# Optimization experiments

Measured on AMD Instinct MI355X. Metric: run time of the kernel, lower is better.

Reference implementation:

```python
import jax, jax.numpy as jnp
import numpy as np

B, P, H, D, CLASSES, L = 2048, 1024, 2048, 256, 10, 10
EP = 1e-64
LOG2PI = float(np.log(2.0 * np.pi))


def setup_inputs() -> dict:
    key = jax.random.key(0)
    ks = jax.random.split(key, 16)
    s = 0.05
    return {
        "data": jax.random.normal(ks[0], (B, P), dtype=jnp.float32),
        "mask": jax.random.randint(ks[1], (B, P), 0, 2) > 0,
        "enc_w1": jax.random.normal(ks[2], (P, H), dtype=jnp.float32) * s,
        "enc_b1": jnp.zeros((H,), jnp.float32),
        "enc_w2": jax.random.normal(ks[3], (H, 2 * D), dtype=jnp.float32) * s,
        "enc_b2": jnp.zeros((2 * D,), jnp.float32),
        "dec_w1": jax.random.normal(ks[4], (D, H), dtype=jnp.float32) * s,
        "dec_b1": jnp.zeros((H,), jnp.float32),
        "dec_w2": jax.random.normal(ks[5], (H, 3 * P), dtype=jnp.float32) * s,
        "dec_b2": jnp.zeros((3 * P,), jnp.float32),
        "cls_w1": jax.random.normal(ks[6], (P, H), dtype=jnp.float32) * s,
        "cls_b1": jnp.zeros((H,), jnp.float32),
        "cls_w2": jax.random.normal(ks[7], (H, CLASSES), dtype=jnp.float32) * s,
        "cls_b2": jnp.zeros((CLASSES,), jnp.float32),
    }


def _student_t_logprob(x, loc, scale, df):
    y = (x - loc) / scale
    return (jax.lax.lgamma((df + 1.0) * 0.5) - jax.lax.lgamma(df * 0.5)
            - 0.5 * jnp.log(df * jnp.pi) - jnp.log(scale)
            - 0.5 * (df + 1.0) * jnp.log1p(y * y / df))


def reference(data, mask, enc_w1, enc_b1, enc_w2, enc_b2,
              dec_w1, dec_b1, dec_w2, dec_b2,
              cls_w1, cls_b1, cls_w2, cls_b2):
    maskf = mask.astype(data.dtype)
    key = jax.random.key(42)
    k_eps, k_t = jax.random.split(key)

    # encoder
    he = jax.nn.relu(data @ enc_w1 + enc_b1)
    out_enc = he @ enc_w2 + enc_b2                      # [B, 2D]
    mu, sig = out_enc[:, :D], jax.nn.softplus(out_enc[:, D:]) + EP

    # reparameterized q(z|x) samples, L draws
    eps = jax.random.normal(k_eps, (L, B, D), dtype=data.dtype)
    z = mu[None] + sig[None] * eps                      # [L, B, D]
    zf = z.reshape(L * B, D)

    # decoder -> StudentT params
    hd = jax.nn.relu(zf @ dec_w1 + dec_b1)
    out_dec = hd @ dec_w2 + dec_b2                      # [L*B, 3P]
    means = out_dec[:, :P]
    scales = jax.nn.softplus(out_dec[:, P:2 * P]) + 0.001
    dfree = jax.nn.softplus(out_dec[:, 2 * P:]) + 3.0

    data_t = jnp.tile(data, (L, 1))                     # [L*B, P]
    mask_t = jnp.tile(maskf, (L, 1))
    logpx = _student_t_logprob(data_t, means, scales, dfree)
    logpxobs = jnp.sum(logpx * mask_t, axis=1).reshape(L, B)

    logpz = jnp.sum(-0.5 * z * z, axis=-1) - 0.5 * D * LOG2PI          # [L, B]
    logq = jnp.sum(-0.5 * eps * eps - jnp.log(sig)[None], axis=-1) - 0.5 * D * LOG2PI

    imp_w = jax.nn.softmax(logpxobs + logpz - logq, axis=0)            # [L, B]

    # non-reparameterized StudentT sample (torch .sample() is detached)
    t = jax.random.t(k_t, dfree, shape=dfree.shape)
    xms = jax.lax.stop_gradient(means + scales * t).reshape(L, B, P)
    xm = jnp.einsum('ki,kij->ij', imp_w, xms)

    data_imputed = jnp.where(mask, data, xm)
    hc = jax.nn.relu(data_imputed @ cls_w1 + cls_b1)
    logits = hc @ cls_w2 + cls_b2
    return (data_imputed, logits)
```

## Files before the change

kernel.cpp:

```cpp
#include <hip/hip_runtime.h>
#include <math.h>

typedef unsigned int u32;
typedef unsigned short u16;
typedef __attribute__((ext_vector_type(8))) short bf16x8;
typedef __attribute__((ext_vector_type(16))) float f32x16;

struct U2 { u32 a, b; };

__host__ __device__ __forceinline__ U2 tf2x32(u32 k0, u32 k1, u32 c0, u32 c1) {
  u32 ks2 = k0 ^ k1 ^ 0x1BD11BDAu;
  u32 x0 = c0 + k0, x1 = c1 + k1;
#define TFR(r) { x0 += x1; x1 = (x1 << (r)) | (x1 >> (32 - (r))); x1 ^= x0; }
  TFR(13) TFR(15) TFR(26) TFR(6)
  x0 += k1; x1 += ks2 + 1u;
  TFR(17) TFR(29) TFR(16) TFR(24)
  x0 += ks2; x1 += k0 + 2u;
  TFR(13) TFR(15) TFR(26) TFR(6)
  x0 += k0; x1 += k1 + 3u;
  TFR(17) TFR(29) TFR(16) TFR(24)
  x0 += k1; x1 += ks2 + 4u;
  TFR(13) TFR(15) TFR(26) TFR(6)
  x0 += ks2; x1 += k0 + 5u;
#undef TFR
  return {x0, x1};
}

__host__ __device__ __forceinline__ u32 prf32(u32 k0, u32 k1, u32 i) {
  U2 r = tf2x32(k0, k1, 0u, i);
  return r.a ^ r.b;
}

__device__ __forceinline__ float u01_from_bits(u32 bits) {
  u32 r = (bits >> 9) | 0x3f800000u;
  return __uint_as_float(r) - 1.0f;
}

__device__ __forceinline__ float erfinv_f32(float x) {
  float w = -log1pf(-x * x);
  float p;
  if (w < 5.0f) {
    w -= 2.5f;
    p = 2.81022636e-08f;
    p = fmaf(p, w, 3.43273939e-07f);
    p = fmaf(p, w, -3.5233877e-06f);
    p = fmaf(p, w, -4.39150654e-06f);
    p = fmaf(p, w, 0.00021858087f);
    p = fmaf(p, w, -0.00125372503f);
    p = fmaf(p, w, -0.00417768164f);
    p = fmaf(p, w, 0.246640727f);
    p = fmaf(p, w, 1.50140941f);
  } else {
    w = sqrtf(w) - 3.0f;
    p = -0.000200214257f;
    p = fmaf(p, w, 0.000100950558f);
    p = fmaf(p, w, 0.00134934322f);
    p = fmaf(p, w, -0.00367342844f);
    p = fmaf(p, w, 0.00573950773f);
    p = fmaf(p, w, -0.0076224613f);
    p = fmaf(p, w, 0.00943887047f);
    p = fmaf(p, w, 1.00167406f);
    p = fmaf(p, w, 2.83297682f);
  }
  return p * x;
}

__device__ __forceinline__ float normal_from_bits(u32 bits) {
  const float lo = -0.99999994f;
  float u = u01_from_bits(bits) * 2.0f + lo;
  u = fmaxf(lo, u);
  return 1.41421356237f * erfinv_f32(u);
}

__device__ __forceinline__ float softplus_f(float x) {
  return fmaxf(x, 0.0f) + log1pf(expf(-fabsf(x)));
}

struct GI { bool acc; float V; u32 k0, k1; };
__device__ __forceinline__ GI gamma_iter(u32 k0, u32 k1, float d, float c) {
  U2 nk = tf2x32(k0, k1, 0u, 0u);
  U2 xk = tf2x32(k0, k1, 0u, 1u);
  U2 uk = tf2x32(k0, k1, 0u, 2u);
  u32 xk0 = xk.a, xk1 = xk.b;
  float x, v;
  do {
    U2 nxt = tf2x32(xk0, xk1, 0u, 0u);
    U2 sub = tf2x32(xk0, xk1, 0u, 1u);
    xk0 = nxt.a; xk1 = nxt.b;
    x = normal_from_bits(prf32(sub.a, sub.b, 0u));
    v = 1.0f + x * c;
  } while (v <= 0.0f);
  float X = x * x;
  float V = (v * v) * v;
  float U = u01_from_bits(prf32(uk.a, uk.b, 0u));
  bool cont = (U >= 1.0f - 0.0331f * (X * X)) &&
              (logf(U) >= 0.5f * X + d * ((1.0f - V) + logf(V)));
  GI r; r.acc = !cont; r.V = V; r.k0 = nk.a; r.k1 = nk.b;
  return r;
}

__device__ __forceinline__ float lgamma_half_diff(float x) {
  float z = x + 3.0f;
  float num = x * (x + 1.0f) * (x + 2.0f);
  float den = (x + 0.5f) * (x + 1.5f) * (x + 2.5f);
  float zh = z + 0.5f;
  float iz = 1.0f / z, izh = 1.0f / zh;
  float corr = 0.0833333333f * (izh - iz)
             - 0.00277777778f * (izh * izh * izh - iz * iz * iz);
  return logf(num / den) + 0.5f * logf(z) + z * log1pf(0.5f * iz) - 0.5f + corr;
}

__device__ __forceinline__ u16 f2bf(float f) {
  u32 u = __float_as_uint(f);
  u32 r = ((u >> 16) & 1u) + 0x7fffu;
  return (u16)((u + r) >> 16);
}
__device__ __forceinline__ float bf2f(u16 h) { return __uint_as_float(((u32)h) << 16); }

__device__ __forceinline__ void split2(float v, u16& h, u16& m) {
  h = f2bf(v);
  m = f2bf(v - bf2f(h));
}

#define GLOAD16(gp, lp) __builtin_amdgcn_global_load_lds( \
    (const __attribute__((address_space(1))) void*)(gp),  \
    (__attribute__((address_space(3))) void*)(lp), 16, 0, 0)

template<bool RELU, bool SIX, bool SWZ>
__global__ __launch_bounds__(256, 4) void gemm_s3(const u16* __restrict__ A2,
                                                  const u16* __restrict__ B2T,
                                                  const float* __restrict__ bias,
                                                  float* __restrict__ Cf,
                                                  u16* __restrict__ C2,
                                                  int N, int kbits) {
  __shared__ u16 As[128 * 64];
  __shared__ u16 Bs[128 * 64];
  const int tid = threadIdx.x;
  const int l = tid & 63, w = tid >> 6;
  int bx = blockIdx.x, by = blockIdx.y;
  if (SWZ) {
    int nx = gridDim.x;
    int wg = by * nx + bx;
    int per = (nx * gridDim.y) >> 3;
    int sw = (wg & 7) * per + (wg >> 3);
    bx = sw % nx; by = sw / nx;
  }
  const int m0 = by * 128, n0 = bx * 128;
  const int K2 = 2 << kbits;
  const int srow = l >> 3;
  const int scol = ((l & 7) ^ srow) << 3;
  const u16* agr[4]; const u16* bgr[4]; u16* al[4]; u16* bl[4];
#pragma unroll
  for (int j = 0; j < 4; ++j) {
    int r = w * 32 + j * 8 + srow;
    agr[j] = A2 + (size_t)(m0 + r) * K2 + scol;
    bgr[j] = B2T + (size_t)(n0 + r) * K2 + scol;
    al[j] = &As[(w * 4 + j) * 512];
    bl[j] = &Bs[(w * 4 + j) * 512];
  }
  f32x16 acc[2][2] = {};
  const int fr = l & 31;
  const int wm = w >> 1, wn = w & 1;
  const int swz = (l & 7) << 4;
  const int hk16 = (l >> 5) << 4;
  const int nk = 3 << (kbits - 6);
  const int kmask = (1 << kbits) - 1;
  for (int kt = 0; kt < nk; ++kt) {
    int vb = kt << 6;
    int s = vb >> kbits;
    int ko = vb & kmask;
    int ao = ((s >> 1) << kbits) + ko;
    int bo = ((s & 1) << kbits) + ko;
    __syncthreads();
#pragma unroll
    for (int j = 0; j < 4; ++j) {
      GLOAD16(agr[j] + ao, al[j]);
      GLOAD16(bgr[j] + bo, bl[j]);
    }
    __syncthreads();
#pragma unroll
    for (int ks = 0; ks < 4; ++ks) {
      bf16x8 af[2], bf[2];
#pragma unroll
      for (int mi = 0; mi < 2; ++mi) {
        int ar = wm * 64 + mi * 32 + fr;
        af[mi] = *(const bf16x8*)((const char*)As + ar * 128 + ((ks * 32 + hk16) ^ swz));
      }
#pragma unroll
      for (int ni = 0; ni < 2; ++ni) {
        int br = wn * 64 + ni * 32 + fr;
        bf[ni] = *(const bf16x8*)((const char*)Bs + br * 128 + ((ks * 32 + hk16) ^ swz));
      }
#pragma unroll
      for (int mi = 0; mi < 2; ++mi)
#pragma unroll
        for (int ni = 0; ni < 2; ++ni)
          acc[mi][ni] = __builtin_amdgcn_mfma_f32_32x32x16_bf16(af[mi], bf[ni], acc[mi][ni], 0, 0, 0);
    }
  }
#pragma unroll
  for (int mi = 0; mi < 2; ++mi)
#pragma unroll
  for (int ni = 0; ni < 2; ++ni) {
    int gcol = n0 + wn * 64 + ni * 32 + fr;
    float bsv = bias[gcol];
#pragma unroll
    for (int r = 0; r < 16; ++r) {
      int grow = m0 + wm * 64 + mi * 32 + (r & 3) + 8 * (r >> 2) + 4 * (l >> 5);
      float v = acc[mi][ni][r] + bsv;
      if (RELU) v = fmaxf(v, 0.0f);
      if (!SIX) {
        Cf[(size_t)grow * N + gcol] = v;
      } else {
        u16 h, mm; split2(v, h, mm);
        u16* q = C2 + (size_t)grow * 2 * N + gcol;
        q[0] = h; q[N] = mm;
      }
    }
  }
}

__global__ __launch_bounds__(256) void k_wconv(const float* __restrict__ W, u16* __restrict__ W2T,
                                               int K, int N) {
  __shared__ float t[64][65];
  const int k0 = blockIdx.y * 64, n0 = blockIdx.x * 64;
  const int tid = threadIdx.x;
  for (int i = tid; i < 4096; i += 256) {
    int kk = i >> 6, nn = i & 63;
    t[kk][nn] = W[(size_t)(k0 + kk) * N + (n0 + nn)];
  }
  __syncthreads();
  const int nn = tid >> 2, kc = (tid & 3) << 4;
  u16* base = W2T + (size_t)(n0 + nn) * 2 * K + (k0 + kc);
#pragma unroll
  for (int kk = 0; kk < 16; ++kk) {
    u16 h, m; split2(t[kc + kk][nn], h, m);
    base[kk] = h; base[K + kk] = m;
  }
}

__global__ __launch_bounds__(256) void k_aconv(const float* __restrict__ X, u16* __restrict__ X2,
                                               int total, int kbits) {
  int i = blockIdx.x * 256 + threadIdx.x;
  if (i >= total) return;
  int K = 1 << kbits;
  int r = i >> kbits, k = i & (K - 1);
  u16 h, m; split2(X[i], h, m);
  u16* q = X2 + ((size_t)r * 2 << kbits) + k;
  q[0] = h; q[K] = m;
}

__global__ __launch_bounds__(256) void k_build(const int* __restrict__ mask,
                                               u16* __restrict__ lists,
                                               int* __restrict__ nmiss) {
  const int b = blockIdx.x, tid = threadIdx.x;
  const int* mrow = mask + b * 1024;
  const int pb = tid * 4;
  int m0 = (mrow[pb] == 0), m1 = (mrow[pb + 1] == 0),
      m2 = (mrow[pb + 2] == 0), m3 = (mrow[pb + 3] == 0);
  int cnt = m0 + m1 + m2 + m3;
  __shared__ int sc[256];
  sc[tid] = cnt;
  __syncthreads();
  for (int off = 1; off < 256; off <<= 1) {
    int v = 0;
    if (tid >= off) v = sc[tid - off];
    __syncthreads();
    sc[tid] += v;
    __syncthreads();
  }
  int pos = sc[tid] - cnt;
  int nmT = sc[255];
  u16* lr = lists + b * 1024;
  int mpos = pos;
  int opos = nmT + (pb - pos);
  if (m0) lr[mpos++] = (u16)pb;       else lr[opos++] = (u16)pb;
  if (m1) lr[mpos++] = (u16)(pb + 1); else lr[opos++] = (u16)(pb + 1);
  if (m2) lr[mpos++] = (u16)(pb + 2); else lr[opos++] = (u16)(pb + 2);
  if (m3) lr[mpos++] = (u16)(pb + 3); else lr[opos++] = (u16)(pb + 3);
  if (tid == 255) nmiss[b] = nmT;
}

__global__ __launch_bounds__(256) void k_eps_z(const float* __restrict__ out_enc,
                                               u16* __restrict__ z2all,
                                               float* __restrict__ logpz,
                                               float* __restrict__ logq,
                                               u32 ke0, u32 ke1) {
  const int lb = blockIdx.x;
  const int b = lb & 2047;
  const int d = threadIdx.x;
  const u32 m = ((u32)lb << 8) + (u32)d;
  float mu = out_enc[b * 512 + d];
  float sg = softplus_f(out_enc[b * 512 + 256 + d]);
  float e = normal_from_bits(prf32(ke0, ke1, m));
  float zz = mu + sg * e;
  u16 h, mm; split2(zz, h, mm);
  u16* q = z2all + (size_t)lb * 512 + d;
  q[0] = h; q[256] = mm;
  float t1 = -0.5f * e * e - logf(sg);
  float t2 = -0.5f * zz * zz;
#pragma unroll
  for (int o = 32; o; o >>= 1) { t1 += __shfl_down(t1, o); t2 += __shfl_down(t2, o); }
  __shared__ float sm1[4], sm2[4];
  int lane = d & 63, wv = d >> 6;
  if (!lane) { sm1[wv] = t1; sm2[wv] = t2; }
  __syncthreads();
  if (d == 0) {
    float a = sm1[0] + sm1[1] + sm1[2] + sm1[3];
    float qq = sm2[0] + sm2[1] + sm2[2] + sm2[3];
    logq[lb]  = a - 235.2482645003962f;
    logpz[lb] = qq - 235.2482645003962f;
  }
}

__global__ __launch_bounds__(256) void k_post(const float* __restrict__ odec,
                                              const float* __restrict__ data,
                                              const u16* __restrict__ lists,
                                              const int* __restrict__ nmiss,
                                              float* __restrict__ lpxobs,
                                              u16* __restrict__ xms,
                                              int l0, u32 kn0, u32 kn1, u32 kg0, u32 kg1) {
  const int row = blockIdx.x;
  const int lb = l0 * 2048 + row;
  const int b = row & 2047;
  const int tid = threadIdx.x;
  const int nm = nmiss[b];
  __shared__ u32 qk0[1024], qk1[1024];
  __shared__ u16 qp[1024];
  __shared__ int qn;
  __shared__ float sm[4];
  if (tid == 0) qn = 0;
  const u16* orow = lists + b * 1024 + nm;
  const int no = 1024 - nm;
  float lpsum = 0.0f;
  for (int t = tid; t < no; t += 256) {
    int p = orow[t];
    float mean  = odec[(size_t)row * 3072 + p];
    float scale = softplus_f(odec[(size_t)row * 3072 + 1024 + p]) + 0.001f;
    float dfv   = softplus_f(odec[(size_t)row * 3072 + 2048 + p]) + 3.0f;
    float x = data[b * 1024 + p];
    float y = (x - mean) / scale;
    lpsum += lgamma_half_diff(dfv * 0.5f)
           - 0.5f * logf(dfv * 3.14159274f) - logf(scale)
           - 0.5f * (dfv + 1.0f) * log1pf(y * y / dfv);
  }
#pragma unroll
  for (int o = 32; o; o >>= 1) lpsum += __shfl_down(lpsum, o);
  int lane = tid & 63, wv = tid >> 6;
  if (!lane) sm[wv] = lpsum;
  __syncthreads();
  if (tid == 0) lpxobs[lb] = sm[0] + sm[1] + sm[2] + sm[3];
  const u16* mr = lists + b * 1024;
  for (int t = tid; t < nm; t += 256) {
    int p = mr[t];
    float mean  = odec[(size_t)row * 3072 + p];
    float scale = softplus_f(odec[(size_t)row * 3072 + 1024 + p]) + 0.001f;
    float dfv   = softplus_f(odec[(size_t)row * 3072 + 2048 + p]) + 3.0f;
    u32 i = ((u32)lb << 10) + (u32)p;
    float n = normal_from_bits(prf32(kn0, kn1, i));
    U2 gk = tf2x32(kg0, kg1, 0u, i);
    U2 kk = tf2x32(gk.a, gk.b, 0u, 0u);
    float half_df = dfv * 0.5f;
    float d = half_df - 0.33333334f;
    float c = 0.33333334f / sqrtf(d);
    GI r = gamma_iter(kk.a, kk.b, d, c);
    if (r.acc) {
      float g = d * r.V;
      xms[i] = f2bf(mean + scale * (n * sqrtf(half_df / g)));
    } else {
      int s = atomicAdd(&qn, 1);
      qk0[s] = r.k0; qk1[s] = r.k1; qp[s] = (u16)p;
    }
  }
  __syncthreads();
  int n2 = qn;
  for (int t = tid; t < n2; t += 256) {
    int p = qp[t];
    float mean  = odec[(size_t)row * 3072 + p];
    float scale = softplus_f(odec[(size_t)row * 3072 + 1024 + p]) + 0.001f;
    float dfv   = softplus_f(odec[(size_t)row * 3072 + 2048 + p]) + 3.0f;
    u32 i = ((u32)lb << 10) + (u32)p;
    float n = normal_from_bits(prf32(kn0, kn1, i));
    float half_df = dfv * 0.5f;
    float d = half_df - 0.33333334f;
    float c = 0.33333334f / sqrtf(d);
    u32 k0 = qk0[t], k1 = qk1[t];
    GI r;
    do { r = gamma_iter(k0, k1, d, c); k0 = r.k0; k1 = r.k1; } while (!r.acc);
    float g = d * r.V;
    xms[i] = f2bf(mean + scale * (n * sqrtf(half_df / g)));
  }
}

__global__ __launch_bounds__(256) void k_impw(const float* __restrict__ lpx,
                                              const float* __restrict__ lpz,
                                              const float* __restrict__ lq,
                                              float* __restrict__ w) {
  int b = blockIdx.x * 256 + threadIdx.x;
  float s[10], mx = -INFINITY;
#pragma unroll
  for (int l = 0; l < 10; ++l) {
    s[l] = lpx[l * 2048 + b] + lpz[l * 2048 + b] - lq[l * 2048 + b];
    mx = fmaxf(mx, s[l]);
  }
  float se = 0.0f;
#pragma unroll
  for (int l = 0; l < 10; ++l) { s[l] = expf(s[l] - mx); se += s[l]; }
#pragma unroll
  for (int l = 0; l < 10; ++l) w[l * 2048 + b] = s[l] / se;
}

__global__ __launch_bounds__(256) void k_xm(const int* __restrict__ mask,
                                            const float* __restrict__ data,
                                            const float* __restrict__ impw,
                                            const u16* __restrict__ xms,
                                            u16* __restrict__ imp2,
                                            float* __restrict__ out) {
  int idx = blockIdx.x * 256 + threadIdx.x;
  int b = idx >> 10, p = idx & 1023;
  float o;
  if (mask[idx]) {
    o = data[idx];
  } else {
    float acc = 0.0f;
#pragma unroll
    for (int l = 0; l < 10; ++l)
      acc += impw[l * 2048 + b] * bf2f(xms[((size_t)l * 2048 + b) * 1024 + p]);
    o = acc;
  }
  out[idx] = o;
  u16 h, m; split2(o, h, m);
  u16* q = imp2 + (size_t)b * 2048 + p;
  q[0] = h; q[1024] = m;
}

__global__ __launch_bounds__(256) void k_cls2(const float* __restrict__ hc,
                                              const float* __restrict__ w2,
                                              const float* __restrict__ b2,
                                              float* __restrict__ out) {
  int b = blockIdx.x, tid = threadIdx.x;
  float acc[10];
#pragma unroll
  for (int c = 0; c < 10; ++c) acc[c] = 0.0f;
  for (int k = tid; k < 2048; k += 256) {
    float h = hc[(size_t)b * 2048 + k];
#pragma unroll
    for (int c = 0; c < 10; ++c) acc[c] = fmaf(h, w2[k * 10 + c], acc[c]);
  }
  __shared__ float red[4][10];
  int lane = tid & 63, wv = tid >> 6;
#pragma unroll
  for (int c = 0; c < 10; ++c) {
    float v = acc[c];
#pragma unroll
    for (int o = 32; o; o >>= 1) v += __shfl_down(v, o);
    if (!lane) red[wv][c] = v;
  }
  __syncthreads();
  if (tid < 10) out[b * 10 + tid] = red[0][tid] + red[1][tid] + red[2][tid] + red[3][tid] + b2[tid];
}

extern "C" void kernel_launch(void* const* d_in, const int* in_sizes, int n_in,
                              void* d_out, int out_size, void* d_ws, size_t ws_size,
                              hipStream_t stream) {
  const float* data   = (const float*)d_in[0];
  const int*   mask   = (const int*)d_in[1];
  const float* enc_w1 = (const float*)d_in[2];
  const float* enc_b1 = (const float*)d_in[3];
  const float* enc_w2 = (const float*)d_in[4];
  const float* enc_b2 = (const float*)d_in[5];
  const float* dec_w1 = (const float*)d_in[6];
  const float* dec_b1 = (const float*)d_in[7];
  const float* dec_w2 = (const float*)d_in[8];
  const float* dec_b2 = (const float*)d_in[9];
  const float* cls_w1 = (const float*)d_in[10];
  const float* cls_b1 = (const float*)d_in[11];
  const float* cls_w2 = (const float*)d_in[12];
  const float* cls_b2 = (const float*)d_in[13];

  float* out = (float*)d_out;
  char* wsb = (char*)d_ws;

  if (ws_size < 207953920ULL) return;

  u16*   xmsu   = (u16*)(wsb + 0);
  u16*   w_d2   = (u16*)(wsb + 41943040);
  u16*   w_d1   = (u16*)(wsb + 67108864);
  u16*   hx2    = (u16*)(wsb + 69206016);
  float* odec   = (float*)(wsb + 102760448);
  u16*   data2  = (u16*)(wsb + 157286400);
  u16*   w_ec   = (u16*)(wsb + 165675008);
  u16*   w_e2   = (u16*)(wsb + 174063616);
  float* logpz  = (float*)(wsb + 178257920);
  float* logq   = (float*)(wsb + 178339840);
  float* lpxobs = (float*)(wsb + 178421760);
  float* impw   = (float*)(wsb + 178503680);
  float* out_enc= (float*)(wsb + 178585600);
  u16*   lists  = (u16*)(wsb + 182779904);
  int*   nmiss  = (int*)(wsb + 186974208);
  u16*   z2all  = (u16*)(wsb + 186982400);
  float* hc     = odec;
  u16*   imp2   = data2;

  U2 ke = tf2x32(0u, 42u, 0u, 0u);
  U2 kt = tf2x32(0u, 42u, 0u, 1u);
  U2 kn = tf2x32(kt.a, kt.b, 0u, 0u);
  U2 kg = tf2x32(kt.a, kt.b, 0u, 1u);

  dim3 blk(256);
  k_aconv<<<8192, blk, 0, stream>>>(data, data2, 2097152, 10);
  k_wconv<<<dim3(32, 16), blk, 0, stream>>>(enc_w1, w_ec, 1024, 2048);
  k_wconv<<<dim3(8, 32),  blk, 0, stream>>>(enc_w2, w_e2, 2048, 512);
  k_wconv<<<dim3(48, 32), blk, 0, stream>>>(dec_w2, w_d2, 2048, 3072);
  k_wconv<<<dim3(32, 4),  blk, 0, stream>>>(dec_w1, w_d1, 256, 2048);
  k_build<<<2048, blk, 0, stream>>>(mask, lists, nmiss);

  gemm_s3<true,  true,  false><<<dim3(16, 16), blk, 0, stream>>>(data2, w_ec, enc_b1, nullptr, hx2, 2048, 10);
  gemm_s3<false, false, false><<<dim3(4, 16),  blk, 0, stream>>>(hx2, w_e2, enc_b2, out_enc, nullptr, 512, 11);

  k_eps_z<<<20480, blk, 0, stream>>>(out_enc, z2all, logpz, logq, ke.a, ke.b);

  for (int l0 = 0; l0 < 10; l0 += 2) {
    gemm_s3<true,  true,  false><<<dim3(16, 32), blk, 0, stream>>>(z2all + (size_t)l0 * 2048 * 512, w_d1, dec_b1, nullptr, hx2, 2048, 8);
    gemm_s3<false, false, true ><<<dim3(24, 32), blk, 0, stream>>>(hx2, w_d2, dec_b2, odec, nullptr, 3072, 11);
    k_post<<<4096, blk, 0, stream>>>(odec, data, lists, nmiss, lpxobs, xmsu, l0, kn.a, kn.b, kg.a, kg.b);
  }

  k_impw<<<8, blk, 0, stream>>>(lpxobs, logpz, logq, impw);
  k_xm<<<8192, blk, 0, stream>>>(mask, data, impw, xmsu, imp2, out);

  k_wconv<<<dim3(32, 16), blk, 0, stream>>>(cls_w1, w_ec, 1024, 2048);
  gemm_s3<true, false, false><<<dim3(16, 16), blk, 0, stream>>>(imp2, w_ec, cls_b1, hc, nullptr, 2048, 10);
  k_cls2<<<2048, blk, 0, stream>>>(hc, cls_w2, cls_b2, out + 2048 * 1024);
}
```

Baseline: 1.843 ms.

## Split-K the encoder and classifier GEMMs with a separate reduction kernel

Adds a split-K mode to the bf16x3 GEMM. Each z-slice of the grid handles a range of K tiles and writes fp32 partials, and a new reduction kernel sums them, adds bias, applies ReLU and splits to bf16 pairs. It is applied to the two encoder GEMMs and the first classifier GEMM, whose 256- and 64-block grids underfill the GPU, in exchange for extra partial-buffer traffic and extra launches. k_eps_z is also changed to one wavefront per row, which removes shared memory and block syncs.

```diff
diff --git a/kernel.cpp b/kernel.cpp
--- a/kernel.cpp
+++ b/kernel.cpp
@@ -126,13 +126,13 @@
     (const __attribute__((address_space(1))) void*)(gp),  \
     (__attribute__((address_space(3))) void*)(lp), 16, 0, 0)
 
-template<bool RELU, bool SIX, bool SWZ>
+template<bool RELU, bool SIX, bool SWZ, bool PARTIAL>
 __global__ __launch_bounds__(256, 4) void gemm_s3(const u16* __restrict__ A2,
                                                   const u16* __restrict__ B2T,
                                                   const float* __restrict__ bias,
                                                   float* __restrict__ Cf,
                                                   u16* __restrict__ C2,
-                                                  int N, int kbits) {
+                                                  int N, int kbits, int tpp) {
   __shared__ u16 As[128 * 64];
   __shared__ u16 Bs[128 * 64];
   const int tid = threadIdx.x;
@@ -163,9 +163,15 @@
   const int wm = w >> 1, wn = w & 1;
   const int swz = (l & 7) << 4;
   const int hk16 = (l >> 5) << 4;
-  const int nk = 3 << (kbits - 6);
+  int kt0 = 0, ktend = 3 << (kbits - 6);
+  float* CfW = Cf;
+  if (PARTIAL) {
+    kt0 = blockIdx.z * tpp;
+    ktend = kt0 + tpp;
+    CfW = Cf + (size_t)blockIdx.z * ((size_t)gridDim.y * 128) * N;
+  }
   const int kmask = (1 << kbits) - 1;
-  for (int kt = 0; kt < nk; ++kt) {
+  for (int kt = kt0; kt < ktend; ++kt) {
     int vb = kt << 6;
     int s = vb >> kbits;
     int ko = vb & kmask;
@@ -203,20 +209,41 @@
 #pragma unroll
   for (int ni = 0; ni < 2; ++ni) {
     int gcol = n0 + wn * 64 + ni * 32 + fr;
-    float bsv = bias[gcol];
+    float bsv = PARTIAL ? 0.0f : bias[gcol];
 #pragma unroll
     for (int r = 0; r < 16; ++r) {
       int grow = m0 + wm * 64 + mi * 32 + (r & 3) + 8 * (r >> 2) + 4 * (l >> 5);
       float v = acc[mi][ni][r] + bsv;
       if (RELU) v = fmaxf(v, 0.0f);
-      if (!SIX) {
-        Cf[(size_t)grow * N + gcol] = v;
+      if (PARTIAL || !SIX) {
+        CfW[(size_t)grow * N + gcol] = v;
       } else {
         u16 h, mm; split2(v, h, mm);
         u16* q = C2 + (size_t)grow * 2 * N + gcol;
         q[0] = h; q[N] = mm;
       }
     }
+  }
+}
+
+template<bool RELU, bool SIX>
+__global__ __launch_bounds__(256) void k_red(const float* __restrict__ P, int NP,
+                                             size_t pstride, const float* __restrict__ bias,
+                                             float* __restrict__ Cf, u16* __restrict__ C2,
+                                             int nbits) {
+  int idx = blockIdx.x * 256 + threadIdx.x;
+  int N = 1 << nbits;
+  int row = idx >> nbits, col = idx & (N - 1);
+  float v = 0.0f;
+  for (int p = 0; p < NP; ++p) v += P[(size_t)p * pstride + idx];
+  v += bias[col];
+  if (RELU) v = fmaxf(v, 0.0f);
+  if (!SIX) {
+    Cf[idx] = v;
+  } else {
+    u16 h, m; split2(v, h, m);
+    C2[(size_t)row * 2 * N + col] = h;
+    C2[(size_t)row * 2 * N + N + col] = m;
   }
 }
 
@@ -286,30 +313,29 @@
                                                float* __restrict__ logpz,
                                                float* __restrict__ logq,
                                                u32 ke0, u32 ke1) {
-  const int lb = blockIdx.x;
+  const int lb = blockIdx.x * 4 + (threadIdx.x >> 6);
+  const int lane = threadIdx.x & 63;
   const int b = lb & 2047;
-  const int d = threadIdx.x;
-  const u32 m = ((u32)lb << 8) + (u32)d;
-  float mu = out_enc[b * 512 + d];
-  float sg = softplus_f(out_enc[b * 512 + 256 + d]);
-  float e = normal_from_bits(prf32(ke0, ke1, m));
-  float zz = mu + sg * e;
-  u16 h, mm; split2(zz, h, mm);
-  u16* q = z2all + (size_t)lb * 512 + d;
-  q[0] = h; q[256] = mm;
-  float t1 = -0.5f * e * e - logf(sg);
-  float t2 = -0.5f * zz * zz;
+  float t1 = 0.0f, t2 = 0.0f;
+  u16* zrow = z2all + (size_t)lb * 512;
+#pragma unroll
+  for (int j = 0; j < 4; ++j) {
+    int d = lane + j * 64;
+    u32 m = ((u32)lb << 8) + (u32)d;
+    float mu = out_enc[b * 512 + d];
+    float sg = softplus_f(out_enc[b * 512 + 256 + d]);
+    float e = normal_from_bits(prf32(ke0, ke1, m));
+    float zz = mu + sg * e;
+    u16 h, mm; split2(zz, h, mm);
+    zrow[d] = h; zrow[256 + d] = mm;
+    t1 += -0.5f * e * e - logf(sg);
+    t2 += -0.5f * zz * zz;
+  }
 #pragma unroll
   for (int o = 32; o; o >>= 1) { t1 += __shfl_down(t1, o); t2 += __shfl_down(t2, o); }
-  __shared__ float sm1[4], sm2[4];
-  int lane = d & 63, wv = d >> 6;
-  if (!lane) { sm1[wv] = t1; sm2[wv] = t2; }
-  __syncthreads();
-  if (d == 0) {
-    float a = sm1[0] + sm1[1] + sm1[2] + sm1[3];
-    float qq = sm2[0] + sm2[1] + sm2[2] + sm2[3];
-    logq[lb]  = a - 235.2482645003962f;
-    logpz[lb] = qq - 235.2482645003962f;
+  if (lane == 0) {
+    logq[lb]  = t1 - 235.2482645003962f;
+    logpz[lb] = t2 - 235.2482645003962f;
   }
 }
 
@@ -501,6 +527,9 @@
   u16*   z2all  = (u16*)(wsb + 186982400);
   float* hc     = odec;
   u16*   imp2   = data2;
+  float* penc1  = odec;
+  float* penc2  = (float*)z2all;
+  float* pcls   = (float*)wsb;
 
   U2 ke = tf2x32(0u, 42u, 0u, 0u);
   U2 kt = tf2x32(0u, 42u, 0u, 1u);
@@ -515,14 +544,16 @@
   k_wconv<<<dim3(32, 4),  blk, 0, stream>>>(dec_w1, w_d1, 256, 2048);
   k_build<<<2048, blk, 0, stream>>>(mask, lists, nmiss);
 
-  gemm_s3<true,  true,  false><<<dim3(16, 16), blk, 0, stream>>>(data2, w_ec, enc_b1, nullptr, hx2, 2048, 10);
-  gemm_s3<false, false, false><<<dim3(4, 16),  blk, 0, stream>>>(hx2, w_e2, enc_b2, out_enc, nullptr, 512, 11);
-
-  k_eps_z<<<20480, blk, 0, stream>>>(out_enc, z2all, logpz, logq, ke.a, ke.b);
+  gemm_s3<false, false, false, true><<<dim3(16, 16, 3), blk, 0, stream>>>(data2, w_ec, enc_b1, penc1, nullptr, 2048, 10, 16);
+  k_red<true, true><<<16384, blk, 0, stream>>>(penc1, 3, (size_t)2048 * 2048, enc_b1, nullptr, hx2, 11);
+  gemm_s3<false, false, false, true><<<dim3(4, 16, 4), blk, 0, stream>>>(hx2, w_e2, enc_b2, penc2, nullptr, 512, 11, 24);
+  k_red<false, false><<<4096, blk, 0, stream>>>(penc2, 4, (size_t)2048 * 512, enc_b2, out_enc, nullptr, 9);
+
+  k_eps_z<<<5120, blk, 0, stream>>>(out_enc, z2all, logpz, logq, ke.a, ke.b);
 
   for (int l0 = 0; l0 < 10; l0 += 2) {
-    gemm_s3<true,  true,  false><<<dim3(16, 32), blk, 0, stream>>>(z2all + (size_t)l0 * 2048 * 512, w_d1, dec_b1, nullptr, hx2, 2048, 8);
-    gemm_s3<false, false, true ><<<dim3(24, 32), blk, 0, stream>>>(hx2, w_d2, dec_b2, odec, nullptr, 3072, 11);
+    gemm_s3<true,  true,  false, false><<<dim3(16, 32), blk, 0, stream>>>(z2all + (size_t)l0 * 2048 * 512, w_d1, dec_b1, nullptr, hx2, 2048, 8, 0);
+    gemm_s3<false, false, true,  false><<<dim3(24, 32), blk, 0, stream>>>(hx2, w_d2, dec_b2, odec, nullptr, 3072, 11, 0);
     k_post<<<4096, blk, 0, stream>>>(odec, data, lists, nmiss, lpxobs, xmsu, l0, kn.a, kn.b, kg.a, kg.b);
   }
 
@@ -530,6 +561,7 @@
   k_xm<<<8192, blk, 0, stream>>>(mask, data, impw, xmsu, imp2, out);
 
   k_wconv<<<dim3(32, 16), blk, 0, stream>>>(cls_w1, w_ec, 1024, 2048);
-  gemm_s3<true, false, false><<<dim3(16, 16), blk, 0, stream>>>(imp2, w_ec, cls_b1, hc, nullptr, 2048, 10);
+  gemm_s3<false, false, false, true><<<dim3(16, 16, 3), blk, 0, stream>>>(imp2, w_ec, cls_b1, pcls, nullptr, 2048, 10, 16);
+  k_red<true, false><<<16384, blk, 0, stream>>>(pcls, 3, (size_t)2048 * 2048, cls_b1, hc, nullptr, 11);
   k_cls2<<<2048, blk, 0, stream>>>(hc, cls_w2, cls_b2, out + 2048 * 1024);
 }
```

Result: faster. 1.786 ms (median of 2 runs) (-3.1%).
